# Kernel tuning notes

Hardware: AMD Instinct MI355X
Metric: run time of the kernel (lower is better)

The kernel has to match this reference:

```python
import jax, jax.numpy as jnp
import numpy as np

N = 50000   # n_nodes (cells)
E = 800000  # n_edges (avg degree 16)
D = 128     # feature dim


def setup_inputs() -> dict:
    key = jax.random.key(0)
    ks = jax.random.split(key, 8)
    x = jax.random.normal(ks[0], (N, D), dtype=jnp.float32)
    src = jax.random.randint(ks[1], (E,), 0, N, dtype=jnp.int32)
    dst = jax.random.randint(ks[2], (E,), 0, N, dtype=jnp.int32)
    vals = jax.random.uniform(ks[3], (E,), dtype=jnp.float32)
    # GraphConvolution weight (dim -> dim), applied as x @ W
    W_gc = jax.random.normal(ks[4], (D, D), dtype=jnp.float32) / np.sqrt(D).astype(np.float32)
    b_gc = jnp.zeros((D,), jnp.float32)
    # linear2: nn.Linear(dim, dim) -> x @ W2.T + b2
    W2 = jax.random.normal(ks[5], (D, D), dtype=jnp.float32) / np.sqrt(D).astype(np.float32)
    b2 = jnp.zeros((D,), jnp.float32)
    return {"x": x, "vals": vals, "W_gc": W_gc, "b_gc": b_gc,
            "W2": W2, "b2": b2, "src": src, "dst": dst}


def reference(x, vals, W_gc, b_gc, W2, b2, src, dst):
    # GraphConvolution (dropout is identity in eval mode):
    #   support = x @ W + b ; out = relu(adj_sparse @ support)
    support = x @ W_gc + b_gc                         # [N, D]
    msg = support[src] * vals[:, None]                # gather rows, scale by edge weight
    agg = jax.ops.segment_sum(msg, dst, num_segments=N)  # SpMM via scatter-add
    x1 = jax.nn.relu(agg)                             # [N, D]
    # linear2 + dropout(eval=identity) + detached L2 row-normalize
    x2 = x1 @ W2.T + b2                               # [N, D]
    nrm = jax.lax.stop_gradient(
        jnp.sqrt(jnp.sum(x2 * x2, axis=1, keepdims=True)))
    return x2 / nrm
```

## Files before the change

### kernel.cpp

```cpp
#include <hip/hip_runtime.h>
#include <hip/hip_bf16.h>

#define N_NODES 50000
#define N_EDGES 800000
#define DIM     128
#define N_STRIPS (N_NODES / 16)
#define N_BKT    ((N_NODES + 255) / 256)
#define EDGE_BLOCKS ((N_EDGES + 4095) / 4096)
#define BUF_CAP  6144
#define GEMM_BLOCKS ((N_STRIPS + 3) / 4)
#define HIST_BLOCK0 GEMM_BLOCKS
#define PACK_BLOCK0 (GEMM_BLOCKS + EDGE_BLOCKS)
#define FRONT_BLOCKS (PACK_BLOCK0 + 8)
#define CHUNKS_PER_PART (EDGE_BLOCKS / 4)

typedef short short8 __attribute__((ext_vector_type(8)));
typedef float floatx4 __attribute__((ext_vector_type(4)));

__device__ inline unsigned short f2bf(float f) {
    __hip_bfloat16 h = __float2bfloat16(f);
    return *reinterpret_cast<unsigned short*>(&h);
}

__global__ __launch_bounds__(256) void pack_w1(
    const float* __restrict__ W, uint4* __restrict__ p1)
{
    const int s    = blockIdx.x * 256 + threadIdx.x;
    const int lane = s & 63;
    const int nt   = (s >> 6) & 7;
    const int ks   = s >> 9;
    const int m    = lane & 15;
    const int q    = lane >> 4;
    unsigned short e[8];
    #pragma unroll
    for (int j = 0; j < 8; ++j)
        e[j] = f2bf(W[(ks * 32 + q * 8 + j) * DIM + nt * 16 + m]);
    uint4 o;
    o.x = (unsigned)e[0] | ((unsigned)e[1] << 16);
    o.y = (unsigned)e[2] | ((unsigned)e[3] << 16);
    o.z = (unsigned)e[4] | ((unsigned)e[5] << 16);
    o.w = (unsigned)e[6] | ((unsigned)e[7] << 16);
    p1[s] = o;
}

__global__ __launch_bounds__(256) void fused_front(
    const float* __restrict__ x, const float* __restrict__ W2,
    const float* __restrict__ bias, const int* __restrict__ dst,
    const uint4* __restrict__ p1,
    unsigned short* __restrict__ support, int* __restrict__ blk_hist,
    uint4* __restrict__ p2)
{
    __shared__ int bh[256];
    const int t = threadIdx.x;

    if (blockIdx.x < HIST_BLOCK0) {
        const int wave  = t >> 6;
        const int lane  = t & 63;
        const int strip = blockIdx.x * 4 + wave;
        if (strip >= N_STRIPS) return;
        const int m = lane & 15;
        const int q = lane >> 4;
        const int row = strip * 16 + m;

        short8 a[4];
        const float4* xr = reinterpret_cast<const float4*>(&x[(size_t)row * DIM]);
        #pragma unroll
        for (int ks = 0; ks < 4; ++ks) {
            const float4 f0 = xr[ks * 8 + q * 2];
            const float4 f1 = xr[ks * 8 + q * 2 + 1];
            short8 tt;
            tt[0] = (short)f2bf(f0.x); tt[1] = (short)f2bf(f0.y);
            tt[2] = (short)f2bf(f0.z); tt[3] = (short)f2bf(f0.w);
            tt[4] = (short)f2bf(f1.x); tt[5] = (short)f2bf(f1.y);
            tt[6] = (short)f2bf(f1.z); tt[7] = (short)f2bf(f1.w);
            a[ks] = tt;
        }

        floatx4 acc[8];
        #pragma unroll
        for (int nt = 0; nt < 8; ++nt) { acc[nt][0]=0.f; acc[nt][1]=0.f; acc[nt][2]=0.f; acc[nt][3]=0.f; }

        const short8* Bp = (const short8*)p1;
        #pragma unroll
        for (int ks = 0; ks < 4; ++ks) {
            #pragma unroll
            for (int nt = 0; nt < 8; ++nt) {
                const short8 bf = Bp[(ks * 8 + nt) * 64 + lane];
                acc[nt] = __builtin_amdgcn_mfma_f32_16x16x32_bf16(a[ks], bf, acc[nt], 0, 0, 0);
            }
        }

        #pragma unroll
        for (int nt = 0; nt < 8; ++nt) {
            const float bb = bias[nt * 16 + m];
            #pragma unroll
            for (int i = 0; i < 4; ++i) {
                const int r = strip * 16 + q * 4 + i;
                support[(size_t)r * DIM + nt * 16 + m] = f2bf(acc[nt][i] + bb);
            }
        }
    } else if (blockIdx.x < PACK_BLOCK0) {
        const int chunk = blockIdx.x - HIST_BLOCK0;
        bh[t] = 0;
        __syncthreads();
        const int base   = chunk * 4096;
        const int navail = min(4096, N_EDGES - base);
        const int4* d4 = reinterpret_cast<const int4*>(dst + base);
        #pragma unroll
        for (int i = 0; i < 4; ++i) {
            const int j = t + i * 256;
            if (j * 4 < navail) {
                const int4 d = d4[j];
                atomicAdd(&bh[d.x >> 8], 1);
                atomicAdd(&bh[d.y >> 8], 1);
                atomicAdd(&bh[d.z >> 8], 1);
                atomicAdd(&bh[d.w >> 8], 1);
            }
        }
        __syncthreads();
        blk_hist[chunk * 256 + t] = bh[t];
    } else {
        const int pb   = blockIdx.x - PACK_BLOCK0;
        const int s    = pb * 256 + t;
        const int lane = s & 63;
        const int nt   = (s >> 6) & 7;
        const int ks   = s >> 9;
        const int m    = lane & 15;
        const int q    = lane >> 4;
        const float4 f0 = *reinterpret_cast<const float4*>(&W2[(nt * 16 + m) * DIM + ks * 32 + q * 8]);
        const float4 f1 = *reinterpret_cast<const float4*>(&W2[(nt * 16 + m) * DIM + ks * 32 + q * 8 + 4]);
        unsigned short e[8];
        e[0] = f2bf(f0.x); e[1] = f2bf(f0.y); e[2] = f2bf(f0.z); e[3] = f2bf(f0.w);
        e[4] = f2bf(f1.x); e[5] = f2bf(f1.y); e[6] = f2bf(f1.z); e[7] = f2bf(f1.w);
        uint4 o;
        o.x = (unsigned)e[0] | ((unsigned)e[1] << 16);
        o.y = (unsigned)e[2] | ((unsigned)e[3] << 16);
        o.z = (unsigned)e[4] | ((unsigned)e[5] << 16);
        o.w = (unsigned)e[6] | ((unsigned)e[7] << 16);
        p2[s] = o;
    }
}

__global__ __launch_bounds__(1024) void scan_hist(
    const int* __restrict__ blk_hist, int* __restrict__ blk_base,
    int* __restrict__ bbase)
{
    __shared__ int psum[4][256];
    __shared__ int stot[256];
    __shared__ int sinc[256];

    const int t    = threadIdx.x;
    const int b    = t & 255;
    const int part = t >> 8;
    const int c0   = part * CHUNKS_PER_PART;

    int pre[CHUNKS_PER_PART];
    int run = 0;
    #pragma unroll
    for (int k = 0; k < CHUNKS_PER_PART; ++k) {
        const int v = blk_hist[(c0 + k) * 256 + b];
        pre[k] = run;
        run += v;
    }
    psum[part][b] = run;
    __syncthreads();

    if (part == 0) {
        const int tot = psum[0][b] + psum[1][b] + psum[2][b] + psum[3][b];
        stot[b] = tot;
        sinc[b] = tot;
    }
    __syncthreads();
    for (int off = 1; off < 256; off <<= 1) {
        int u = 0;
        if (part == 0 && b >= off) u = sinc[b - off];
        __syncthreads();
        if (part == 0 && b >= off) sinc[b] += u;
        __syncthreads();
    }
    const int ex = sinc[b] - stot[b];
    if (part == 0 && b < N_BKT) bbase[b] = ex;
    if (t == 0) bbase[N_BKT] = N_EDGES;

    int partbase = 0;
    #pragma unroll
    for (int p = 0; p < 4; ++p) if (p < part) partbase += psum[p][b];
    const int add = ex + partbase;
    #pragma unroll
    for (int k = 0; k < CHUNKS_PER_PART; ++k)
        blk_base[(c0 + k) * 256 + b] = pre[k] + add;
}

__global__ __launch_bounds__(256) void bucket_scatter(
    const int* __restrict__ src, const int* __restrict__ dst,
    const float* __restrict__ vals, const int* __restrict__ blk_base,
    int2* __restrict__ bucketed)
{
    __shared__ int rcur[256];
    const int t     = threadIdx.x;
    const int chunk = blockIdx.x;
    rcur[t] = blk_base[chunk * 256 + t];
    __syncthreads();

    const int base   = chunk * 4096;
    const int navail = min(4096, N_EDGES - base);
    const int4*   s4 = reinterpret_cast<const int4*>(src + base);
    const int4*   d4 = reinterpret_cast<const int4*>(dst + base);
    const float4* v4 = reinterpret_cast<const float4*>(vals + base);
    #pragma unroll
    for (int i = 0; i < 4; ++i) {
        const int j = t + i * 256;
        if (j * 4 < navail) {
            const int4   s = s4[j];
            const int4   d = d4[j];
            const float4 v = v4[j];
            int p;
            p = atomicAdd(&rcur[d.x >> 8], 1);
            bucketed[p] = make_int2((s.x & 0xFFFF) | ((d.x & 0xFF) << 16), __float_as_int(v.x));
            p = atomicAdd(&rcur[d.y >> 8], 1);
            bucketed[p] = make_int2((s.y & 0xFFFF) | ((d.y & 0xFF) << 16), __float_as_int(v.y));
            p = atomicAdd(&rcur[d.z >> 8], 1);
            bucketed[p] = make_int2((s.z & 0xFFFF) | ((d.z & 0xFF) << 16), __float_as_int(v.z));
            p = atomicAdd(&rcur[d.w >> 8], 1);
            bucketed[p] = make_int2((s.w & 0xFFFF) | ((d.w & 0xFF) << 16), __float_as_int(v.w));
        }
    }
}

__global__ __launch_bounds__(512) void bucket_to_csr(
    const int2* __restrict__ bucketed, const int* __restrict__ bbase,
    int2* __restrict__ packed, int* __restrict__ offs)
{
    __shared__ int cnt[256];
    __shared__ int sc[256];
    __shared__ int lcur[256];
    __shared__ int2 buf[BUF_CAP];

    const int b    = blockIdx.x;
    const int t    = threadIdx.x;
    const int base = bbase[b];
    const int nE   = bbase[b + 1] - base;

    if (t < 256) cnt[t] = 0;
    __syncthreads();
    for (int i = t; i < nE; i += 512)
        atomicAdd(&cnt[(bucketed[base + i].x >> 16) & 0xFF], 1);
    __syncthreads();
    if (t < 256) sc[t] = cnt[t];
    __syncthreads();
    #pragma unroll
    for (int off = 1; off < 256; off <<= 1) {
        int u = 0;
        if (t < 256 && t >= off) u = sc[t - off];
        __syncthreads();
        if (t < 256 && t >= off) sc[t] += u;
        __syncthreads();
    }
    if (t < 256) lcur[t] = sc[t] - cnt[t];
    __syncthreads();

    if (nE <= BUF_CAP) {
        for (int i = t; i < nE; i += 512) {
            const int2 e = bucketed[base + i];
            const int  n = (e.x >> 16) & 0xFF;
            const int  p = atomicAdd(&lcur[n], 1);
            buf[p] = make_int2(e.x & 0xFFFF, e.y);
        }
        __syncthreads();
        for (int i = t; i < nE; i += 512)
            packed[base + i] = buf[i];
    } else {
        for (int i = t; i < nE; i += 512) {
            const int2 e = bucketed[base + i];
            const int  n = (e.x >> 16) & 0xFF;
            const int  p = atomicAdd(&lcur[n], 1);
            packed[base + p] = make_int2(e.x & 0xFFFF, e.y);
        }
    }

    if (t < 256) {
        const int node = b * 256 + t;
        if (node < N_NODES) offs[node] = base + (sc[t] - cnt[t]);
    }
    if (b == N_BKT - 1 && t == 0) offs[N_NODES] = N_EDGES;
}

__global__ __launch_bounds__(256) void csr_gather_bf16(
    const unsigned int* __restrict__ sup, const int2* __restrict__ packed,
    const int* __restrict__ offs, unsigned int* __restrict__ agg)
{
    const int node = (blockIdx.x * 256 + threadIdx.x) >> 6;
    const int lane = threadIdx.x & 63;
    if (node >= N_NODES) return;
    const int beg = offs[node];
    const int end = offs[node + 1];

    float ax = 0.f, ay = 0.f;
    int j = beg;
    for (; j + 7 < end; j += 8) {
        int2 e[8];
        unsigned int u[8];
        #pragma unroll
        for (int k = 0; k < 8; ++k) e[k] = packed[j + k];
        #pragma unroll
        for (int k = 0; k < 8; ++k) u[k] = sup[(size_t)e[k].x * 64 + lane];
        #pragma unroll
        for (int k = 0; k < 8; ++k) {
            const float v = __int_as_float(e[k].y);
            ax += __uint_as_float(u[k] << 16) * v;
            ay += __uint_as_float(u[k] & 0xffff0000u) * v;
        }
    }
    for (; j + 3 < end; j += 4) {
        int2 e[4];
        unsigned int u[4];
        #pragma unroll
        for (int k = 0; k < 4; ++k) e[k] = packed[j + k];
        #pragma unroll
        for (int k = 0; k < 4; ++k) u[k] = sup[(size_t)e[k].x * 64 + lane];
        #pragma unroll
        for (int k = 0; k < 4; ++k) {
            const float v = __int_as_float(e[k].y);
            ax += __uint_as_float(u[k] << 16) * v;
            ay += __uint_as_float(u[k] & 0xffff0000u) * v;
        }
    }
    for (; j < end; ++j) {
        const int2 e0 = packed[j];
        const unsigned int u0 = sup[(size_t)e0.x * 64 + lane];
        const float v0 = __int_as_float(e0.y);
        ax += __uint_as_float(u0 << 16) * v0;
        ay += __uint_as_float(u0 & 0xffff0000u) * v0;
    }
    ax = fmaxf(ax, 0.f);
    ay = fmaxf(ay, 0.f);
    agg[(size_t)node * 64 + lane] = (unsigned int)f2bf(ax) | ((unsigned int)f2bf(ay) << 16);
}

__global__ __launch_bounds__(256) void gemm2_mfma(
    const short8* __restrict__ aggv, const short8* __restrict__ Bp,
    const float* __restrict__ bias, float* __restrict__ out)
{
    const int wave  = threadIdx.x >> 6;
    const int lane  = threadIdx.x & 63;
    const int strip = blockIdx.x * 4 + wave;
    if (strip >= N_STRIPS) return;
    const int m = lane & 15;
    const int q = lane >> 4;
    const int row = strip * 16 + m;

    short8 a[4];
    #pragma unroll
    for (int ks = 0; ks < 4; ++ks)
        a[ks] = aggv[(size_t)row * (DIM / 8) + ks * 4 + q];

    floatx4 acc[8];
    #pragma unroll
    for (int nt = 0; nt < 8; ++nt) { acc[nt][0]=0.f; acc[nt][1]=0.f; acc[nt][2]=0.f; acc[nt][3]=0.f; }

    #pragma unroll
    for (int ks = 0; ks < 4; ++ks) {
        #pragma unroll
        for (int nt = 0; nt < 8; ++nt) {
            const short8 bf = Bp[(ks * 8 + nt) * 64 + lane];
            acc[nt] = __builtin_amdgcn_mfma_f32_16x16x32_bf16(a[ks], bf, acc[nt], 0, 0, 0);
        }
    }

    #pragma unroll
    for (int nt = 0; nt < 8; ++nt) {
        const float bb = bias[nt * 16 + m];
        #pragma unroll
        for (int i = 0; i < 4; ++i) acc[nt][i] += bb;
    }

    float sq[4] = {0.f, 0.f, 0.f, 0.f};
    #pragma unroll
    for (int nt = 0; nt < 8; ++nt)
        #pragma unroll
        for (int i = 0; i < 4; ++i) sq[i] += acc[nt][i] * acc[nt][i];
    #pragma unroll
    for (int i = 0; i < 4; ++i) {
        #pragma unroll
        for (int mask = 1; mask < 16; mask <<= 1)
            sq[i] += __shfl_xor(sq[i], mask);
        sq[i] = 1.0f / sqrtf(sq[i]);
    }

    #pragma unroll
    for (int nt = 0; nt < 8; ++nt) {
        #pragma unroll
        for (int i = 0; i < 4; ++i) {
            const int r = strip * 16 + q * 4 + i;
            out[(size_t)r * DIM + nt * 16 + m] = acc[nt][i] * sq[i];
        }
    }
}

extern "C" void kernel_launch(void* const* d_in, const int* in_sizes, int n_in,
                              void* d_out, int out_size, void* d_ws, size_t ws_size,
                              hipStream_t stream) {
    const float* x    = (const float*)d_in[0];
    const float* vals = (const float*)d_in[1];
    const float* W_gc = (const float*)d_in[2];
    const float* b_gc = (const float*)d_in[3];
    const float* W2   = (const float*)d_in[4];
    const float* b2   = (const float*)d_in[5];
    const int*   src  = (const int*)d_in[6];
    const int*   dst  = (const int*)d_in[7];

    unsigned short* support = (unsigned short*)d_out;
    float* out = (float*)d_out;

    const size_t AGG_B  = (size_t)N_NODES * DIM * 2;
    const size_t OFFS_B = 200064;
    const size_t BH_B   = (size_t)EDGE_BLOCKS * 256 * 4;
    const size_t BB_B   = (size_t)EDGE_BLOCKS * 256 * 4;
    const size_t BKT_B  = 1024;
    const size_t BUK_B  = (size_t)N_EDGES * 8;
    const size_t PACK_B = (size_t)N_EDGES * 8;
    const size_t PW_B   = 32768;

    char* wsb = (char*)d_ws;
    unsigned int* agg = (unsigned int*)wsb;
    int*   offs     = (int*)(wsb + AGG_B);
    int*   blk_hist = (int*)(wsb + AGG_B + OFFS_B);
    int*   blk_base = (int*)(wsb + AGG_B + OFFS_B + BH_B);
    int*   bbase    = (int*)(wsb + AGG_B + OFFS_B + BH_B + BB_B);
    int2*  bucketed = (int2*)(wsb + AGG_B + OFFS_B + BH_B + BB_B + BKT_B);
    int2*  packed   = (int2*)(wsb + AGG_B + OFFS_B + BH_B + BB_B + BKT_B + BUK_B);
    uint4* pw1      = (uint4*)(wsb + AGG_B + OFFS_B + BH_B + BB_B + BKT_B + BUK_B + PACK_B);
    uint4* pw2      = (uint4*)(wsb + AGG_B + OFFS_B + BH_B + BB_B + BKT_B + BUK_B + PACK_B + PW_B);

    pack_w1<<<8, 256, 0, stream>>>(W_gc, pw1);

    fused_front<<<FRONT_BLOCKS, 256, 0, stream>>>(
        x, W2, b_gc, dst, pw1, support, blk_hist, pw2);

    scan_hist<<<1, 1024, 0, stream>>>(blk_hist, blk_base, bbase);

    bucket_scatter<<<EDGE_BLOCKS, 256, 0, stream>>>(src, dst, vals, blk_base, bucketed);

    bucket_to_csr<<<N_BKT, 512, 0, stream>>>(bucketed, bbase, packed, offs);

    csr_gather_bf16<<<(N_NODES * 64 + 255) / 256, 256, 0, stream>>>(
        (const unsigned int*)support, packed, offs, agg);

    gemm2_mfma<<<GEMM_BLOCKS, 256, 0, stream>>>(
        (const short8*)agg, (const short8*)pw2, b2, out);
}
```

Baseline: 164.2 us.

## Merge scan, bucket scatter and CSR build into one cooperative kernel

Replaces three kernels (histogram scan, bucket scatter, bucket-to-CSR) with a single cooperative kernel that uses grid-wide syncs between phases, saving two launch boundaries. Block 0 performs the scan serially over all edge chunks with 256 threads, while the other blocks wait at the grid barrier. This relies on EDGE_BLOCKS equalling N_BKT (196) and on every block being co-resident. Grid.sync costs and the less parallel scan may offset the launch savings.

```diff
diff --git a/kernel.cpp b/kernel.cpp
--- a/kernel.cpp
+++ b/kernel.cpp
@@ -1,5 +1,8 @@
 #include <hip/hip_runtime.h>
 #include <hip/hip_bf16.h>
+#include <hip/hip_cooperative_groups.h>
+
+namespace cg = cooperative_groups;
 
 #define N_NODES 50000
 #define N_EDGES 800000
@@ -12,7 +15,6 @@
 #define HIST_BLOCK0 GEMM_BLOCKS
 #define PACK_BLOCK0 (GEMM_BLOCKS + EDGE_BLOCKS)
 #define FRONT_BLOCKS (PACK_BLOCK0 + 8)
-#define CHUNKS_PER_PART (EDGE_BLOCKS / 4)
 
 typedef short short8 __attribute__((ext_vector_type(8)));
 typedef float floatx4 __attribute__((ext_vector_type(4)));
@@ -141,103 +143,93 @@
     }
 }
 
-__global__ __launch_bounds__(1024) void scan_hist(
-    const int* __restrict__ blk_hist, int* __restrict__ blk_base,
-    int* __restrict__ bbase)
-{
-    __shared__ int psum[4][256];
-    __shared__ int stot[256];
-    __shared__ int sinc[256];
-
-    const int t    = threadIdx.x;
-    const int b    = t & 255;
-    const int part = t >> 8;
-    const int c0   = part * CHUNKS_PER_PART;
-
-    int pre[CHUNKS_PER_PART];
-    int run = 0;
-    #pragma unroll
-    for (int k = 0; k < CHUNKS_PER_PART; ++k) {
-        const int v = blk_hist[(c0 + k) * 256 + b];
-        pre[k] = run;
-        run += v;
-    }
-    psum[part][b] = run;
-    __syncthreads();
-
-    if (part == 0) {
-        const int tot = psum[0][b] + psum[1][b] + psum[2][b] + psum[3][b];
-        stot[b] = tot;
-        sinc[b] = tot;
-    }
-    __syncthreads();
-    for (int off = 1; off < 256; off <<= 1) {
-        int u = 0;
-        if (part == 0 && b >= off) u = sinc[b - off];
-        __syncthreads();
-        if (part == 0 && b >= off) sinc[b] += u;
-        __syncthreads();
-    }
-    const int ex = sinc[b] - stot[b];
-    if (part == 0 && b < N_BKT) bbase[b] = ex;
-    if (t == 0) bbase[N_BKT] = N_EDGES;
-
-    int partbase = 0;
-    #pragma unroll
-    for (int p = 0; p < 4; ++p) if (p < part) partbase += psum[p][b];
-    const int add = ex + partbase;
-    #pragma unroll
-    for (int k = 0; k < CHUNKS_PER_PART; ++k)
-        blk_base[(c0 + k) * 256 + b] = pre[k] + add;
-}
-
-__global__ __launch_bounds__(256) void bucket_scatter(
-    const int* __restrict__ src, const int* __restrict__ dst,
-    const float* __restrict__ vals, const int* __restrict__ blk_base,
-    int2* __restrict__ bucketed)
-{
-    __shared__ int rcur[256];
-    const int t     = threadIdx.x;
-    const int chunk = blockIdx.x;
-    rcur[t] = blk_base[chunk * 256 + t];
-    __syncthreads();
-
-    const int base   = chunk * 4096;
-    const int navail = min(4096, N_EDGES - base);
-    const int4*   s4 = reinterpret_cast<const int4*>(src + base);
-    const int4*   d4 = reinterpret_cast<const int4*>(dst + base);
-    const float4* v4 = reinterpret_cast<const float4*>(vals + base);
-    #pragma unroll
-    for (int i = 0; i < 4; ++i) {
-        const int j = t + i * 256;
-        if (j * 4 < navail) {
-            const int4   s = s4[j];
-            const int4   d = d4[j];
-            const float4 v = v4[j];
-            int p;
-            p = atomicAdd(&rcur[d.x >> 8], 1);
-            bucketed[p] = make_int2((s.x & 0xFFFF) | ((d.x & 0xFF) << 16), __float_as_int(v.x));
-            p = atomicAdd(&rcur[d.y >> 8], 1);
-            bucketed[p] = make_int2((s.y & 0xFFFF) | ((d.y & 0xFF) << 16), __float_as_int(v.y));
-            p = atomicAdd(&rcur[d.z >> 8], 1);
-            bucketed[p] = make_int2((s.z & 0xFFFF) | ((d.z & 0xFF) << 16), __float_as_int(v.z));
-            p = atomicAdd(&rcur[d.w >> 8], 1);
-            bucketed[p] = make_int2((s.w & 0xFFFF) | ((d.w & 0xFF) << 16), __float_as_int(v.w));
-        }
-    }
-}
-
-__global__ __launch_bounds__(512) void bucket_to_csr(
-    const int2* __restrict__ bucketed, const int* __restrict__ bbase,
-    int2* __restrict__ packed, int* __restrict__ offs)
+__global__ __launch_bounds__(512) void csr_coop(
+    const int* __restrict__ blk_hist, const int* __restrict__ src,
+    const int* __restrict__ dst, const float* __restrict__ vals,
+    int* __restrict__ blk_base, int* __restrict__ bbase,
+    int2* __restrict__ bucketed, int2* __restrict__ packed,
+    int* __restrict__ offs)
 {
     __shared__ int cnt[256];
     __shared__ int sc[256];
     __shared__ int lcur[256];
     __shared__ int2 buf[BUF_CAP];
 
-    const int b    = blockIdx.x;
-    const int t    = threadIdx.x;
+    cg::grid_group grid = cg::this_grid();
+    const int b = blockIdx.x;
+    const int t = threadIdx.x;
+
+    if (b == 0) {
+        int tot = 0;
+        if (t < 256) {
+            for (int c = 0; c < EDGE_BLOCKS; c += 4) {
+                const int v0 = blk_hist[(c + 0) * 256 + t];
+                const int v1 = blk_hist[(c + 1) * 256 + t];
+                const int v2 = blk_hist[(c + 2) * 256 + t];
+                const int v3 = blk_hist[(c + 3) * 256 + t];
+                tot += v0 + v1 + v2 + v3;
+            }
+            sc[t] = tot;
+        }
+        __syncthreads();
+        for (int off = 1; off < 256; off <<= 1) {
+            int u = 0;
+            if (t < 256 && t >= off) u = sc[t - off];
+            __syncthreads();
+            if (t < 256 && t >= off) sc[t] += u;
+            __syncthreads();
+        }
+        if (t < 256) {
+            const int ex = sc[t] - tot;
+            if (t < N_BKT) bbase[t] = ex;
+            int run = ex;
+            for (int c = 0; c < EDGE_BLOCKS; c += 4) {
+                const int v0 = blk_hist[(c + 0) * 256 + t];
+                const int v1 = blk_hist[(c + 1) * 256 + t];
+                const int v2 = blk_hist[(c + 2) * 256 + t];
+                const int v3 = blk_hist[(c + 3) * 256 + t];
+                blk_base[(c + 0) * 256 + t] = run;
+                blk_base[(c + 1) * 256 + t] = run + v0;
+                blk_base[(c + 2) * 256 + t] = run + v0 + v1;
+                blk_base[(c + 3) * 256 + t] = run + v0 + v1 + v2;
+                run += v0 + v1 + v2 + v3;
+            }
+        }
+        if (t == 0) bbase[N_BKT] = N_EDGES;
+    }
+    __threadfence();
+    grid.sync();
+
+    if (t < 256) lcur[t] = blk_base[b * 256 + t];
+    __syncthreads();
+    {
+        const int base   = b * 4096;
+        const int navail = min(4096, N_EDGES - base);
+        const int4*   s4 = reinterpret_cast<const int4*>(src + base);
+        const int4*   d4 = reinterpret_cast<const int4*>(dst + base);
+        const float4* v4 = reinterpret_cast<const float4*>(vals + base);
+        #pragma unroll
+        for (int i = 0; i < 2; ++i) {
+            const int j = t + i * 512;
+            if (j * 4 < navail) {
+                const int4   s = s4[j];
+                const int4   d = d4[j];
+                const float4 v = v4[j];
+                int p;
+                p = atomicAdd(&lcur[d.x >> 8], 1);
+                bucketed[p] = make_int2((s.x & 0xFFFF) | ((d.x & 0xFF) << 16), __float_as_int(v.x));
+                p = atomicAdd(&lcur[d.y >> 8], 1);
+                bucketed[p] = make_int2((s.y & 0xFFFF) | ((d.y & 0xFF) << 16), __float_as_int(v.y));
+                p = atomicAdd(&lcur[d.z >> 8], 1);
+                bucketed[p] = make_int2((s.z & 0xFFFF) | ((d.z & 0xFF) << 16), __float_as_int(v.z));
+                p = atomicAdd(&lcur[d.w >> 8], 1);
+                bucketed[p] = make_int2((s.w & 0xFFFF) | ((d.w & 0xFF) << 16), __float_as_int(v.w));
+            }
+        }
+    }
+    __threadfence();
+    grid.sync();
+
     const int base = bbase[b];
     const int nE   = bbase[b + 1] - base;
 
@@ -437,11 +429,15 @@
     fused_front<<<FRONT_BLOCKS, 256, 0, stream>>>(
         x, W2, b_gc, dst, pw1, support, blk_hist, pw2);
 
-    scan_hist<<<1, 1024, 0, stream>>>(blk_hist, blk_base, bbase);
-
-    bucket_scatter<<<EDGE_BLOCKS, 256, 0, stream>>>(src, dst, vals, blk_base, bucketed);
-
-    bucket_to_csr<<<N_BKT, 512, 0, stream>>>(bucketed, bbase, packed, offs);
+    {
+        void* args[] = {
+            (void*)&blk_hist, (void*)&src, (void*)&dst, (void*)&vals,
+            (void*)&blk_base, (void*)&bbase, (void*)&bucketed,
+            (void*)&packed, (void*)&offs
+        };
+        hipLaunchCooperativeKernel((const void*)csr_coop, dim3(N_BKT), dim3(512),
+                                   args, 0, stream);
+    }
 
     csr_gather_bf16<<<(N_NODES * 64 + 255) / 256, 256, 0, stream>>>(
         (const unsigned int*)support, packed, offs, agg);
```

After: 326.3 us. +98.7%, slower.
